# Kernel optimization log

Measured on AMD Instinct MI355X. Metric: run time of the kernel, lower is better.

## Reference

```python
import jax, jax.numpy as jnp
import numpy as np

S, T, B = 32, 64, 64          # sentences, tokens/sentence, batch
V, E, H, G, C = 32000, 128, 128, 128, 5  # vocab, embed, intra hid, inter hid, classes


def _gru_dir(x, h0, Wih, Whh, bih, bhh):
    # x: [T,B,D]; Wih: [3H,D]; Whh: [3H,H]  (PyTorch GRU gate order r,z,n)
    xg = jnp.einsum('tbd,gd->tbg', x, Wih) + bih  # precompute input gates [T,B,3H]
    def step(h, xt):
        gh = h @ Whh.T + bhh
        ir, iz, inn = jnp.split(xt, 3, axis=-1)
        hr, hz, hn = jnp.split(gh, 3, axis=-1)
        r = jax.nn.sigmoid(ir + hr)
        z = jax.nn.sigmoid(iz + hz)
        n = jnp.tanh(inn + r * hn)
        hnew = (1 - z) * n + z * h
        return hnew, hnew
    _, out = jax.lax.scan(step, h0, xg)
    return out  # [T,B,H]


def _bigru(x, Wih, Whh, bih, bhh):
    # x: [T,B,D]; Wih: [2,3H,D] (fwd, bwd). Zero initial state (init_hidden()).
    h0 = jnp.zeros((x.shape[1], Whh.shape[-1]), x.dtype)
    of = _gru_dir(x, h0, Wih[0], Whh[0], bih[0], bhh[0])
    ob = _gru_dir(x[::-1], h0, Wih[1], Whh[1], bih[1], bhh[1])[::-1]
    return jnp.concatenate([of, ob], axis=-1)  # [T,B,2H]


def setup_inputs() -> dict:
    key = jax.random.key(0)
    ks = iter(jax.random.split(key, 20))
    u = lambda k, shp, s: jax.random.uniform(k, shp, jnp.float32, -s, s)
    tokens = jax.random.randint(next(ks), (S, T, B), 0, V)
    return {
        'tokens': tokens,
        'embed_table': jax.random.normal(next(ks), (V, E), jnp.float32),
        # intra biGRU (input E, hidden H)
        'Wih_intra': u(next(ks), (2, 3 * H, E), 0.08),
        'Whh_intra': u(next(ks), (2, 3 * H, H), 0.08),
        'bih_intra': u(next(ks), (2, 3 * H), 0.08),
        'bhh_intra': u(next(ks), (2, 3 * H), 0.08),
        # intra attention
        'W_W_intra': u(next(ks), (2 * H, 2 * H), 0.1),
        'b_intra': u(next(ks), (2 * H,), 0.1),
        'proj_intra': u(next(ks), (2 * H,), 0.1),
        # inter biGRU (input 2H, hidden G)
        'Wih_inter': u(next(ks), (2, 3 * G, 2 * H), 0.08),
        'Whh_inter': u(next(ks), (2, 3 * G, G), 0.08),
        'bih_inter': u(next(ks), (2, 3 * G), 0.08),
        'bhh_inter': u(next(ks), (2, 3 * G), 0.08),
        # inter attention
        'W_W_inter': u(next(ks), (2 * G, 2 * G), 0.1),
        'b_inter': u(next(ks), (2 * G,), 0.1),
        'proj_inter': u(next(ks), (2 * G,), 0.1),
        # final linear
        'W_final': u(next(ks), (C, 2 * G), 0.06),
        'b_final': u(next(ks), (C,), 0.06),
    }


def reference(tokens, embed_table, Wih_intra, Whh_intra, bih_intra, bhh_intra,
              W_W_intra, b_intra, proj_intra, Wih_inter, Whh_inter, bih_inter,
              bhh_inter, W_W_inter, b_inter, proj_inter, W_final, b_final):
    # ---- intra (word-level) per sentence, fresh zero state each sentence ----
    emb = embed_table[tokens]                                   # [S,T,B,E]
    intra_out = jax.vmap(
        lambda xs: _bigru(xs, Wih_intra, Whh_intra, bih_intra, bhh_intra)
    )(emb)                                                      # [S,T,B,2H]
    u1 = jnp.tanh(jnp.einsum('stbh,hk->stbk', intra_out, W_W_intra) + b_intra)
    a1 = jnp.einsum('stbk,k->stb', u1, proj_intra)              # [S,T,B]
    a1 = jax.nn.softmax(a1, axis=1)                             # softmax over tokens
    sent_vecs = jnp.einsum('stb,stbh->sbh', a1, intra_out)      # [S,B,2H]
    # ---- inter (sentence-level) ----
    inter_out = _bigru(sent_vecs, Wih_inter, Whh_inter, bih_inter, bhh_inter)  # [S,B,2G]
    u2 = jnp.tanh(jnp.einsum('sbh,hk->sbk', inter_out, W_W_inter) + b_inter)
    a2 = jnp.einsum('sbk,k->sb', u2, proj_inter)                # NO softmax (faithful to source)
    doc_vec = jnp.einsum('sb,sbh->bh', a2, inter_out)           # [B,2G]
    final_map = doc_vec @ W_final.T + b_final                   # [B,C]
    return final_map
```

## Files before the change

### kernel.cpp

```cpp
#include <hip/hip_runtime.h>

#define S_ 32
#define T_ 64
#define B_ 64
#define V_ 32000
#define E_ 128
#define H_ 128
#define G_ 128
#define C_ 5

typedef short s8v __attribute__((ext_vector_type(8)));
typedef __bf16 b8v __attribute__((ext_vector_type(8)));
typedef float f32x4 __attribute__((ext_vector_type(4)));

template <typename V>
__device__ inline auto mfma_sel(V a, V b, f32x4 c, int)
    -> decltype(__builtin_amdgcn_mfma_f32_16x16x32_bf16(a, b, c, 0, 0, 0)) {
  return __builtin_amdgcn_mfma_f32_16x16x32_bf16(a, b, c, 0, 0, 0);
}
template <typename V>
__device__ inline f32x4 mfma_sel(V a, V b, f32x4 c, long) {
  return __builtin_amdgcn_mfma_f32_16x16x32_bf16(
      __builtin_bit_cast(b8v, a), __builtin_bit_cast(b8v, b), c, 0, 0, 0);
}
__device__ inline f32x4 mfma16(s8v a, s8v b, f32x4 c) { return mfma_sel(a, b, c, 0); }

__device__ inline float b2f(unsigned short u) {
  union { unsigned int i; float f; } v; v.i = ((unsigned int)u) << 16; return v.f;
}
__device__ inline unsigned short f2b(float f) {
  union { float f; unsigned int i; } v; v.f = f;
  return (unsigned short)((v.i + 0x8000u) >> 16);
}
__device__ inline unsigned short f2b_rne(float f) {
  union { float f; unsigned int i; } v; v.f = f;
  unsigned int r = (v.i + 0x7fffu + ((v.i >> 16) & 1u)) >> 16;
  return (unsigned short)r;
}
__device__ inline s8v cvt8(const float* p) {
  const float4 a = *(const float4*)p;
  const float4 b = *(const float4*)(p + 4);
  s8v r;
  r[0] = (short)f2b_rne(a.x); r[1] = (short)f2b_rne(a.y);
  r[2] = (short)f2b_rne(a.z); r[3] = (short)f2b_rne(a.w);
  r[4] = (short)f2b_rne(b.x); r[5] = (short)f2b_rne(b.y);
  r[6] = (short)f2b_rne(b.z); r[7] = (short)f2b_rne(b.w);
  return r;
}
__device__ inline float fsigm(float x) {
  return __builtin_amdgcn_rcpf(1.f + __builtin_amdgcn_exp2f(-1.44269504f * x));
}
__device__ inline float ftanh(float x) {
  return 1.f - 2.f * __builtin_amdgcn_rcpf(1.f + __builtin_amdgcn_exp2f(2.88539008f * x));
}

__device__ inline void lds_barrier() {
  asm volatile("s_waitcnt lgkmcnt(0)\n\ts_barrier" ::: "memory");
}

__global__ __launch_bounds__(256) void k_gtab(
    const float* __restrict__ emb,
    const float* __restrict__ wih,
    const float* __restrict__ bih,
    const float* __restrict__ bhh,
    const float* __restrict__ wwi,
    const float* __restrict__ wihI,
    unsigned short* __restrict__ gtab,
    unsigned short* __restrict__ wta,
    unsigned short* __restrict__ wib)
{
  __shared__ __align__(16) unsigned short res[64 * 776];
  __shared__ __align__(16) unsigned short alds[64 * 136];
  const int bid = blockIdx.x, tid = threadIdx.x;
  if (bid >= 504) {
    const int cb = bid - 504;
    for (int i = 0; i < 48; ++i) {
      int e4 = cb * 12288 + i * 256 + tid;
      float4 v = *(const float4*)&wihI[(size_t)e4 * 4];
      ushort4 u;
      u.x = f2b_rne(v.x); u.y = f2b_rne(v.y); u.z = f2b_rne(v.z); u.w = f2b_rne(v.w);
      *(ushort4*)&wib[(size_t)e4 * 4] = u;
    }
    return;
  }
  if (bid >= 500) {
    const int n0 = (bid - 500) * 64;
    for (int i = 0; i < 64; ++i) {
      int cid = i * 256 + tid;
      int k = cid >> 6, nl = cid & 63;
      res[nl * 264 + k] = f2b_rne(wwi[k * 256 + n0 + nl]);
    }
    __syncthreads();
    for (int i = 0; i < 8; ++i) {
      int cid = i * 256 + tid;
      int nl = cid >> 5, k8 = cid & 31;
      *(int4*)&wta[(size_t)(n0 + nl) * 256 + k8 * 8] =
          *(const int4*)&res[nl * 264 + k8 * 8];
    }
    return;
  }
  const int vbase = bid * 64;
  for (int i = 0; i < 8; ++i) {
    int cid = i * 256 + tid;
    int row = cid >> 5, kc = cid & 31;
    float4 v = *(const float4*)&emb[(size_t)(vbase + row) * 128 + kc * 4];
    ushort4 u;
    u.x = f2b_rne(v.x); u.y = f2b_rne(v.y); u.z = f2b_rne(v.z); u.w = f2b_rne(v.w);
    *(ushort4*)&alds[row * 136 + kc * 4] = u;
  }
  __syncthreads();
  const int w = tid >> 6, l = tid & 63, q = l >> 4, ln = l & 15;
  s8v af[4][4];
  for (int mt = 0; mt < 4; ++mt)
    for (int kf = 0; kf < 4; ++kf)
      af[mt][kf] = *(const s8v*)&alds[(mt * 16 + ln) * 136 + kf * 32 + q * 8];
  for (int nchunk = 0; nchunk < 6; ++nchunk) {
    const int nbase = nchunk * 128;
    s8v bf[2][4];
    float bias[2];
    for (int nt = 0; nt < 2; ++nt) {
      int c = nbase + (w * 2 + nt) * 16 + ln;
      int g = (c < 384) ? c : (c - 384);
      bias[nt] = bih[c] + (g < 256 ? bhh[c] : 0.f);
      for (int kf = 0; kf < 4; ++kf)
        bf[nt][kf] = cvt8(&wih[(size_t)c * 128 + kf * 32 + q * 8]);
    }
    for (int mt = 0; mt < 4; ++mt) {
      for (int nt = 0; nt < 2; ++nt) {
        f32x4 acc = {0.f, 0.f, 0.f, 0.f};
        for (int kf = 0; kf < 4; ++kf) acc = mfma16(af[mt][kf], bf[nt][kf], acc);
        const int col = nbase + (w * 2 + nt) * 16 + ln;
        for (int r = 0; r < 4; ++r) {
          const int row = mt * 16 + q * 4 + r;
          res[row * 776 + col] = f2b_rne(acc[r] + bias[nt]);
        }
      }
    }
  }
  __syncthreads();
  for (int i = 0; i < 24; ++i) {
    int cid = i * 256 + tid;
    int row = cid / 96, kc = cid - row * 96;
    *(int4*)&gtab[(size_t)(vbase + row) * 768 + kc * 8] =
        *(const int4*)&res[row * 776 + kc * 8];
  }
}

__global__ __launch_bounds__(512) void k_intra(
    const int* __restrict__ tokens,
    const unsigned short* __restrict__ gtab,
    const float* __restrict__ whh,
    const float* __restrict__ bhh,
    unsigned short* __restrict__ iout)
{
  const int bid = blockIdx.x;
  const int s = bid >> 3, dir = (bid >> 2) & 1, bq = bid & 3;
  const int bbase = bq * 16;
  const int tid = threadIdx.x;
  const int w = tid >> 6, l = tid & 63, q = l >> 4, ln = l & 15;
  const int gbase = w * 16, g0 = gbase + q * 4;

  __shared__ __align__(16) unsigned short hb[2][16 * 136];
  __shared__ __align__(16) unsigned short xbuf[2][16 * 392];
  __shared__ int tokl[T_ * 16];

  for (int i = tid; i < 2 * 16 * 136; i += 512) ((unsigned short*)hb)[i] = 0;
  for (int i = tid; i < T_ * 16; i += 512) {
    int t = i >> 4, bl = i & 15;
    tokl[i] = tokens[(s * T_ + t) * B_ + bbase + bl] * 768 + dir * 384;
  }

  s8v af[3][4];
  float hbn[4];
  const float* whd = whh + (size_t)dir * (384 * 128);
  const float* bhd = bhh + dir * 384;
  for (int g3 = 0; g3 < 3; ++g3)
    for (int kf = 0; kf < 4; ++kf)
      af[g3][kf] = cvt8(&whd[(size_t)(g3 * 128 + gbase + ln) * 128 + kf * 32 + q * 8]);
  for (int r = 0; r < 4; ++r) hbn[r] = bhd[256 + gbase + q * 4 + r];
  float h[4] = {0.f, 0.f, 0.f, 0.f};

  const bool stager = (w < 6);
  int sr0 = 0, sof0 = 0, sd0 = 0, sr1 = 0, sof1 = 0, sd1 = 0;
  {
    int e0 = w * 1024 + l * 8;
    int e1 = e0 + 512;
    sr0 = e0 / 384; sof0 = e0 - sr0 * 384; sd0 = sr0 * 392 + sof0;
    sr1 = e1 / 384; sof1 = e1 - sr1 * 384; sd1 = sr1 * 392 + sof1;
  }
  int4 ldA, ldB;
#define XLOAD(st)                                                           \
  do {                                                                      \
    int tt_ = (st) > (T_ - 1) ? (T_ - 1) : (st);                            \
    int tg_ = dir ? (T_ - 1 - tt_) : tt_;                                   \
    ldA = *(const int4*)&gtab[(size_t)tokl[tg_ * 16 + sr0] + sof0];         \
    ldB = *(const int4*)&gtab[(size_t)tokl[tg_ * 16 + sr1] + sof1];         \
  } while (0)
#define XWRITE(sl)                                                          \
  do {                                                                      \
    *(int4*)&xbuf[sl][sd0] = ldA;                                           \
    *(int4*)&xbuf[sl][sd1] = ldB;                                           \
  } while (0)

  __syncthreads();
  if (stager) {
    XLOAD(0);
    XWRITE(0);
    XLOAD(1);
  }
  __syncthreads();

  const int xb = ln * 392 + gbase + q * 4;
  int p = 0;
  int tprev = 0;
  for (int step = 0; step < T_; ++step) {
    const int t = dir ? (T_ - 1 - step) : step;
    const int sl = step & 1;
    if (stager) {
      XWRITE(sl ^ 1);
      XLOAD(step + 2);
    }
    if (step > 0 && tid < 256) {
      int row = tid >> 4, kc = tid & 15;
      int4 v = *(const int4*)&hb[p][row * 136 + kc * 8];
      *(int4*)&iout[((size_t)(s * T_ + tprev) * B_ + bbase + row) * 256 +
                    dir * 128 + kc * 8] = v;
    }
    s8v bfr[4];
    for (int kf = 0; kf < 4; ++kf)
      bfr[kf] = *(const s8v*)&hb[p][ln * 136 + kf * 32 + q * 8];
    f32x4 c0 = {0.f, 0.f, 0.f, 0.f}, c1 = c0, c2 = c0;
    for (int kf = 0; kf < 4; ++kf) {
      c0 = mfma16(af[0][kf], bfr[kf], c0);
      c1 = mfma16(af[1][kf], bfr[kf], c1);
      c2 = mfma16(af[2][kf], bfr[kf], c2);
    }
    const ushort4 xr = *(const ushort4*)&xbuf[sl][xb];
    const ushort4 xz = *(const ushort4*)&xbuf[sl][xb + 128];
    const ushort4 xn = *(const ushort4*)&xbuf[sl][xb + 256];
    const unsigned short* xrp = (const unsigned short*)&xr;
    const unsigned short* xzp = (const unsigned short*)&xz;
    const unsigned short* xnp = (const unsigned short*)&xn;
    unsigned short hnb[4];
    for (int r = 0; r < 4; ++r) {
      float rr = fsigm(b2f(xrp[r]) + c0[r]);
      float zz = fsigm(b2f(xzp[r]) + c1[r]);
      float nn = ftanh(b2f(xnp[r]) + rr * (c2[r] + hbn[r]));
      float hv = zz * (h[r] - nn) + nn;
      h[r] = hv;
      hnb[r] = f2b(hv);
    }
    ushort4 hv4; hv4.x = hnb[0]; hv4.y = hnb[1]; hv4.z = hnb[2]; hv4.w = hnb[3];
    *(ushort4*)&hb[p ^ 1][ln * 136 + g0] = hv4;
    lds_barrier();
    p ^= 1;
    tprev = t;
  }
  if (tid < 256) {
    int row = tid >> 4, kc = tid & 15;
    int4 v = *(const int4*)&hb[p][row * 136 + kc * 8];
    *(int4*)&iout[((size_t)(s * T_ + tprev) * B_ + bbase + row) * 256 +
                  dir * 128 + kc * 8] = v;
  }
#undef XLOAD
#undef XWRITE
}

__global__ __launch_bounds__(512, 1) void k_attn(
    const unsigned short* __restrict__ iout,
    const unsigned short* __restrict__ wta,
    const float* __restrict__ bint,
    const float* __restrict__ proj,
    const unsigned short* __restrict__ wib,
    const float* __restrict__ bihI,
    const float* __restrict__ bhhI,
    float* __restrict__ xgi)
{
  __shared__ __align__(16) unsigned short wlds[256 * 256];
  __shared__ float lgbuf[8][16];
  __shared__ float lbuf[8][8];
  const int tid = threadIdx.x, bid = blockIdx.x;
  const int s = bid >> 3, b0 = (bid & 7) * 8;
  for (int i = 0; i < 16; ++i) {
    int cid = i * 512 + tid;
    int n = cid >> 5, kc = cid & 31;
    *(int4*)&wlds[n * 256 + ((kc ^ (n & 15)) << 3)] =
        *(const int4*)&wta[(size_t)n * 256 + kc * 8];
  }
  const int w = tid >> 6, l = tid & 63, q = l >> 4, ln = l & 15;
  float bbv[16], ppv[16];
  for (int nt = 0; nt < 16; ++nt) {
    bbv[nt] = bint[nt * 16 + ln];
    ppv[nt] = proj[nt * 16 + ln];
  }
  __syncthreads();

  float O[8][8];
  for (int kf = 0; kf < 8; ++kf)
    for (int j = 0; j < 8; ++j) O[kf][j] = 0.f;
  float l_acc = 0.f;

  for (int tile = 0; tile < 4; ++tile) {
    const int t = (w * 4 + tile) * 2 + (ln >> 3);
    const size_t row = (size_t)((s * T_ + t) * B_ + b0 + (ln & 7));
    s8v af[8];
    for (int kf = 0; kf < 8; ++kf)
      af[kf] = *(const s8v*)&iout[row * 256 + kf * 32 + q * 8];
    float p0 = 0.f, p1 = 0.f, p2 = 0.f, p3 = 0.f;
    for (int nt = 0; nt < 16; ++nt) {
      f32x4 c = {0.f, 0.f, 0.f, 0.f};
      for (int kf = 0; kf < 8; ++kf) {
        s8v bf = *(const s8v*)&wlds[(nt * 16 + ln) * 256 + (((kf * 4 + q) ^ ln) << 3)];
        c = mfma16(af[kf], bf, c);
      }
      p0 += ppv[nt] * ftanh(c[0] + bbv[nt]);
      p1 += ppv[nt] * ftanh(c[1] + bbv[nt]);
      p2 += ppv[nt] * ftanh(c[2] + bbv[nt]);
      p3 += ppv[nt] * ftanh(c[3] + bbv[nt]);
    }
    for (int d = 1; d < 16; d <<= 1) {
      p0 += __shfl_xor(p0, d); p1 += __shfl_xor(p1, d);
      p2 += __shfl_xor(p2, d); p3 += __shfl_xor(p3, d);
    }
    if (ln == 0) {
      lgbuf[w][q * 4 + 0] = p0; lgbuf[w][q * 4 + 1] = p1;
      lgbuf[w][q * 4 + 2] = p2; lgbuf[w][q * 4 + 3] = p3;
    }
    const float lg = lgbuf[w][ln];
    const float e = __builtin_amdgcn_exp2f(1.44269504f * lg);
    l_acc += e;
    for (int kf = 0; kf < 8; ++kf)
      for (int j = 0; j < 8; ++j)
        O[kf][j] += e * b2f((unsigned short)af[kf][j]);
  }
  l_acc += __shfl_xor(l_acc, 8);
  for (int kf = 0; kf < 8; ++kf)
    for (int j = 0; j < 8; ++j) O[kf][j] += __shfl_xor(O[kf][j], 8);
  __syncthreads();
  float* obuf = (float*)wlds;
  unsigned short* svl = (unsigned short*)(((char*)wlds) + 65536);
  if (ln < 8) {
    const int base = w * 2048 + ln * 256 + q * 8;
    for (int kf = 0; kf < 8; ++kf) {
      float4 v0; v0.x = O[kf][0]; v0.y = O[kf][1]; v0.z = O[kf][2]; v0.w = O[kf][3];
      float4 v1; v1.x = O[kf][4]; v1.y = O[kf][5]; v1.z = O[kf][6]; v1.w = O[kf][7];
      *(float4*)&obuf[base + kf * 32]     = v0;
      *(float4*)&obuf[base + kf * 32 + 4] = v1;
    }
    if (q == 0) lbuf[w][ln] = l_acc;
  }
  {
    ushort4 z4; z4.x = 0; z4.y = 0; z4.z = 0; z4.w = 0;
    int rr = 8 + (tid >> 6), cc = (tid & 63) * 4;
    *(ushort4*)&svl[rr * 264 + cc] = z4;
  }
  __syncthreads();
  const int idx = tid * 4;
  const int bb_ = idx >> 8;
  float4 acc; acc.x = 0.f; acc.y = 0.f; acc.z = 0.f; acc.w = 0.f;
  float lsum = 0.f;
  for (int w8 = 0; w8 < 8; ++w8) {
    const float4 v = *(const float4*)&obuf[w8 * 2048 + idx];
    acc.x += v.x; acc.y += v.y; acc.z += v.z; acc.w += v.w;
    lsum += lbuf[w8][bb_];
  }
  const float inv = __builtin_amdgcn_rcpf(lsum);
  ushort4 u;
  u.x = f2b_rne(acc.x * inv); u.y = f2b_rne(acc.y * inv);
  u.z = f2b_rne(acc.z * inv); u.w = f2b_rne(acc.w * inv);
  *(ushort4*)&svl[bb_ * 264 + (idx & 255)] = u;
  __syncthreads();
  s8v afx[8];
  for (int kf = 0; kf < 8; ++kf)
    afx[kf] = *(const s8v*)&svl[ln * 264 + kf * 32 + q * 8];
  for (int nt = 0; nt < 6; ++nt) {
    const int c = w * 96 + nt * 16 + ln;
    const int dirI = (c >= 384) ? 1 : 0;
    const int g = c - dirI * 384;
    const float biasx = bihI[c] + (g < 256 ? bhhI[c] : 0.f);
    f32x4 cacc = {0.f, 0.f, 0.f, 0.f};
    for (int kf = 0; kf < 8; ++kf) {
      s8v bfx = *(const s8v*)&wib[(size_t)c * 256 + kf * 32 + q * 8];
      cacc = mfma16(afx[kf], bfx, cacc);
    }
    if (q < 2) {
      for (int r = 0; r < 4; ++r) {
        const int m = q * 4 + r;
        xgi[((size_t)dirI * 2048 + s * B_ + b0 + m) * 384 + g] = cacc[r] + biasx;
      }
    }
  }
}

__global__ __launch_bounds__(512) void k_inter(
    const float* __restrict__ xgi,
    const float* __restrict__ whh,
    const float* __restrict__ bhh,
    float* __restrict__ io2)
{
  const int bid = blockIdx.x;
  const int dir = bid >> 2, bq = bid & 3, bbase = bq * 16;
  const int tid = threadIdx.x;
  const int w = tid >> 6, l = tid & 63, q = l >> 4, ln = l & 15;
  const int gbase = w * 16, g0 = gbase + q * 4;
  __shared__ __align__(16) unsigned short hb[2][16 * 136];
  for (int i = tid; i < 2 * 16 * 136; i += 512) ((unsigned short*)hb)[i] = 0;
  s8v af[3][4];
  float hbn[4];
  const float* whd = whh + (size_t)dir * (384 * 128);
  const float* bhd = bhh + dir * 384;
  for (int g3 = 0; g3 < 3; ++g3) {
    const int R = g3 * 128 + gbase;
    for (int kf = 0; kf < 4; ++kf)
      af[g3][kf] = cvt8(&whd[(size_t)(R + ln) * 128 + kf * 32 + q * 8]);
  }
  for (int r = 0; r < 4; ++r) hbn[r] = bhd[256 + gbase + q * 4 + r];
  float h[4] = {0.f, 0.f, 0.f, 0.f};
  const int b = bbase + ln;
  __syncthreads();

  float4 Vr[4], Vz[4], Vn[4];
#define GLOAD_S(slot, st)                                                   \
  do {                                                                      \
    int tt_ = (st) > (S_ - 1) ? (S_ - 1) : (st);                            \
    int sg_ = dir ? (S_ - 1 - tt_) : tt_;                                   \
    const float* xp_ = xgi + ((size_t)dir * 2048 + sg_ * 64 + b) * 384 + g0;\
    Vr[slot] = *(const float4*)&xp_[0];                                     \
    Vz[slot] = *(const float4*)&xp_[128];                                   \
    Vn[slot] = *(const float4*)&xp_[256];                                   \
  } while (0)

  GLOAD_S(0, 0);
  GLOAD_S(1, 1);
  GLOAD_S(2, 2);

  int p = 0;
  for (int it = 0; it < S_ / 4; ++it) {
#pragma unroll
    for (int j = 0; j < 4; ++j) {
      const int step = it * 4 + j;
      const int sI = dir ? (S_ - 1 - step) : step;
      GLOAD_S((j + 3) & 3, step + 3);

      s8v bfr[4];
      for (int kf = 0; kf < 4; ++kf)
        bfr[kf] = *(const s8v*)&hb[p][ln * 136 + kf * 32 + q * 8];
      f32x4 c0 = {0.f, 0.f, 0.f, 0.f}, c1 = c0, c2 = c0;
      for (int kf = 0; kf < 4; ++kf) {
        c0 = mfma16(af[0][kf], bfr[kf], c0);
        c1 = mfma16(af[1][kf], bfr[kf], c1);
        c2 = mfma16(af[2][kf], bfr[kf], c2);
      }
      const float irv[4] = {Vr[j].x, Vr[j].y, Vr[j].z, Vr[j].w};
      const float izv[4] = {Vz[j].x, Vz[j].y, Vz[j].z, Vz[j].w};
      const float inv[4] = {Vn[j].x, Vn[j].y, Vn[j].z, Vn[j].w};
      unsigned short hnb[4];
      for (int r = 0; r < 4; ++r) {
        float rr = fsigm(irv[r] + c0[r]);
        float zz = fsigm(izv[r] + c1[r]);
        float nn = ftanh(inv[r] + rr * (c2[r] + hbn[r]));
        float hv = zz * (h[r] - nn) + nn;
        h[r] = hv;
        hnb[r] = f2b(hv);
      }
      ushort4 hv4; hv4.x = hnb[0]; hv4.y = hnb[1]; hv4.z = hnb[2]; hv4.w = hnb[3];
      *(ushort4*)&hb[p ^ 1][ln * 136 + g0] = hv4;
      float4 of4; of4.x = h[0]; of4.y = h[1]; of4.z = h[2]; of4.w = h[3];
      *(float4*)&io2[((size_t)(sI * 64 + b)) * 256 + dir * 128 + g0] = of4;
      lds_barrier();
      p ^= 1;
    }
  }
#undef GLOAD_S
}

__global__ __launch_bounds__(256) void k_attn_i(
    const float* __restrict__ io2,
    const float* __restrict__ wwI,
    const float* __restrict__ bI,
    const float* __restrict__ projI,
    float* __restrict__ a2)
{
  const int bid = blockIdx.x, tid = threadIdx.x;
  const int r0 = bid * 8;
  __shared__ float iol[8 * 256];
  __shared__ float red[4 * 8];
  for (int i = 0; i < 8; ++i) iol[i * 256 + tid] = io2[(size_t)(r0 + i) * 256 + tid];
  __syncthreads();
  float acc[8];
  for (int i = 0; i < 8; ++i) acc[i] = 0.f;
  for (int hh = 0; hh < 256; ++hh) {
    const float wv = wwI[hh * 256 + tid];
    for (int i = 0; i < 8; ++i) acc[i] += wv * iol[i * 256 + hh];
  }
  const float bb = bI[tid], pp = projI[tid];
  float p[8];
  for (int i = 0; i < 8; ++i) p[i] = pp * ftanh(acc[i] + bb);
  for (int d = 1; d < 64; d <<= 1)
    for (int i = 0; i < 8; ++i) p[i] += __shfl_xor(p[i], d);
  const int w = tid >> 6, l = tid & 63;
  if (l == 0)
    for (int i = 0; i < 8; ++i) red[w * 8 + i] = p[i];
  __syncthreads();
  if (tid < 8) a2[r0 + tid] = red[tid] + red[8 + tid] + red[16 + tid] + red[24 + tid];
}

__global__ __launch_bounds__(256) void k_final(
    const float* __restrict__ a2,
    const float* __restrict__ io2,
    const float* __restrict__ wf,
    const float* __restrict__ bfi,
    float* __restrict__ out)
{
  const int b = blockIdx.x, tid = threadIdx.x;
  __shared__ float av[S_];
  __shared__ float dv[256];
  __shared__ float red[4];
  if (tid < S_) av[tid] = a2[tid * 64 + b];
  __syncthreads();
  float acc = 0.f;
  for (int s = 0; s < S_; ++s) acc += av[s] * io2[((size_t)(s * 64 + b)) * 256 + tid];
  dv[tid] = acc;
  __syncthreads();
  for (int c = 0; c < C_; ++c) {
    float pv = wf[c * 256 + tid] * dv[tid];
    for (int d = 1; d < 64; d <<= 1) pv += __shfl_xor(pv, d);
    const int w = tid >> 6, l = tid & 63;
    if (l == 0) red[w] = pv;
    __syncthreads();
    if (tid == 0)
      out[b * C_ + c] = red[0] + red[1] + red[2] + red[3] + bfi[c];
    __syncthreads();
  }
}

extern "C" void kernel_launch(void* const* d_in, const int* in_sizes, int n_in,
                              void* d_out, int out_size, void* d_ws, size_t ws_size,
                              hipStream_t stream) {
  (void)in_sizes; (void)n_in; (void)out_size; (void)ws_size;
  const int*   tokens = (const int*)d_in[0];
  const float* emb    = (const float*)d_in[1];
  const float* wih_a  = (const float*)d_in[2];
  const float* whh_a  = (const float*)d_in[3];
  const float* bih_a  = (const float*)d_in[4];
  const float* bhh_a  = (const float*)d_in[5];
  const float* ww_a   = (const float*)d_in[6];
  const float* b_a    = (const float*)d_in[7];
  const float* proj_a = (const float*)d_in[8];
  const float* wih_i  = (const float*)d_in[9];
  const float* whh_i  = (const float*)d_in[10];
  const float* bih_i  = (const float*)d_in[11];
  const float* bhh_i  = (const float*)d_in[12];
  const float* ww_i   = (const float*)d_in[13];
  const float* b_i    = (const float*)d_in[14];
  const float* proj_i = (const float*)d_in[15];
  const float* w_fin  = (const float*)d_in[16];
  const float* b_fin  = (const float*)d_in[17];

  char* ws = (char*)d_ws;
  unsigned short* gtab = (unsigned short*)(ws + 0);
  unsigned short* wta  = (unsigned short*)(ws + 49152000);
  unsigned short* iout = (unsigned short*)(ws + 49283072);
  unsigned short* wib  = (unsigned short*)(ws + 116391936);
  float* xgi = (float*)(ws + 119537664);
  float* io2 = (float*)(ws + 125829120);
  float* a2  = (float*)(ws + 127926272);

  k_gtab<<<508, 256, 0, stream>>>(emb, wih_a, bih_a, bhh_a, ww_a, wih_i,
                                  gtab, wta, wib);
  k_intra<<<256, 512, 0, stream>>>(tokens, gtab, whh_a, bhh_a, iout);
  k_attn<<<256, 512, 0, stream>>>(iout, wta, b_a, proj_a, wib, bih_i, bhh_i, xgi);
  k_inter<<<8, 512, 0, stream>>>(xgi, whh_i, bhh_i, io2);
  k_attn_i<<<256, 256, 0, stream>>>(io2, ww_i, b_i, proj_i, a2);
  k_final<<<64, 256, 0, stream>>>(a2, io2, w_fin, b_fin, (float*)d_out);
}
```

Measured before the change: 294.8 us.

## Fuse attention, inter GRU, inter attention and final into one persistent kernel

Merges the four post-intra kernels into a single 256-block kernel that separates stages with software grid barriers built on atomic counters in workspace. The counters are reset by the preceding intra kernel. This removes three kernel launches and their inter-kernel gaps. In exchange it relies on all 256 blocks being co-resident, and it adds spin-wait overhead while 248 blocks idle during the serial inter GRU.

Result: slower. 619.3 us (+110.1%).

```diff
diff --git a/kernel.cpp b/kernel.cpp
--- a/kernel.cpp
+++ b/kernel.cpp
@@ -8,6 +8,7 @@
 #define H_ 128
 #define G_ 128
 #define C_ 5
+#define NB_ 256
 
 typedef short s8v __attribute__((ext_vector_type(8)));
 typedef __bf16 b8v __attribute__((ext_vector_type(8)));
@@ -56,6 +57,17 @@
 
 __device__ inline void lds_barrier() {
   asm volatile("s_waitcnt lgkmcnt(0)\n\ts_barrier" ::: "memory");
+}
+
+__device__ inline void gsync(int* c) {
+  __syncthreads();
+  if (threadIdx.x == 0) {
+    __threadfence();
+    atomicAdd(c, 1);
+    while (atomicAdd(c, 0) < NB_) __builtin_amdgcn_s_sleep(16);
+    __threadfence();
+  }
+  __syncthreads();
 }
 
 __global__ __launch_bounds__(256) void k_gtab(
@@ -151,12 +163,14 @@
     const unsigned short* __restrict__ gtab,
     const float* __restrict__ whh,
     const float* __restrict__ bhh,
-    unsigned short* __restrict__ iout)
+    unsigned short* __restrict__ iout,
+    int* __restrict__ gctr)
 {
   const int bid = blockIdx.x;
   const int s = bid >> 3, dir = (bid >> 2) & 1, bq = bid & 3;
   const int bbase = bq * 16;
   const int tid = threadIdx.x;
+  if (bid == 0 && tid < 4) gctr[tid] = 0;
   const int w = tid >> 6, l = tid & 63, q = l >> 4, ln = l & 15;
   const int gbase = w * 16, g0 = gbase + q * 4;
 
@@ -266,7 +280,7 @@
 #undef XWRITE
 }
 
-__global__ __launch_bounds__(512, 1) void k_attn(
+__global__ __launch_bounds__(512, 1) void k_mega(
     const unsigned short* __restrict__ iout,
     const unsigned short* __restrict__ wta,
     const float* __restrict__ bint,
@@ -274,263 +288,264 @@
     const unsigned short* __restrict__ wib,
     const float* __restrict__ bihI,
     const float* __restrict__ bhhI,
-    float* __restrict__ xgi)
+    float* __restrict__ xgi,
+    const float* __restrict__ whhI,
+    float* __restrict__ io2,
+    const float* __restrict__ wwI,
+    const float* __restrict__ bI,
+    const float* __restrict__ projI,
+    const float* __restrict__ wf,
+    const float* __restrict__ bfi,
+    float* __restrict__ a2,
+    int* __restrict__ gctr,
+    float* __restrict__ out)
 {
   __shared__ __align__(16) unsigned short wlds[256 * 256];
   __shared__ float lgbuf[8][16];
   __shared__ float lbuf[8][8];
   const int tid = threadIdx.x, bid = blockIdx.x;
-  const int s = bid >> 3, b0 = (bid & 7) * 8;
-  for (int i = 0; i < 16; ++i) {
-    int cid = i * 512 + tid;
-    int n = cid >> 5, kc = cid & 31;
-    *(int4*)&wlds[n * 256 + ((kc ^ (n & 15)) << 3)] =
-        *(const int4*)&wta[(size_t)n * 256 + kc * 8];
-  }
-  const int w = tid >> 6, l = tid & 63, q = l >> 4, ln = l & 15;
-  float bbv[16], ppv[16];
-  for (int nt = 0; nt < 16; ++nt) {
-    bbv[nt] = bint[nt * 16 + ln];
-    ppv[nt] = proj[nt * 16 + ln];
-  }
-  __syncthreads();
-
-  float O[8][8];
-  for (int kf = 0; kf < 8; ++kf)
-    for (int j = 0; j < 8; ++j) O[kf][j] = 0.f;
-  float l_acc = 0.f;
-
-  for (int tile = 0; tile < 4; ++tile) {
-    const int t = (w * 4 + tile) * 2 + (ln >> 3);
-    const size_t row = (size_t)((s * T_ + t) * B_ + b0 + (ln & 7));
-    s8v af[8];
+
+  {
+    const int s = bid >> 3, b0 = (bid & 7) * 8;
+    for (int i = 0; i < 16; ++i) {
+      int cid = i * 512 + tid;
+      int n = cid >> 5, kc = cid & 31;
+      *(int4*)&wlds[n * 256 + ((kc ^ (n & 15)) << 3)] =
+          *(const int4*)&wta[(size_t)n * 256 + kc * 8];
+    }
+    const int w = tid >> 6, l = tid & 63, q = l >> 4, ln = l & 15;
+    float bbv[16], ppv[16];
+    for (int nt = 0; nt < 16; ++nt) {
+      bbv[nt] = bint[nt * 16 + ln];
+      ppv[nt] = proj[nt * 16 + ln];
+    }
+    __syncthreads();
+
+    float O[8][8];
     for (int kf = 0; kf < 8; ++kf)
-      af[kf] = *(const s8v*)&iout[row * 256 + kf * 32 + q * 8];
-    float p0 = 0.f, p1 = 0.f, p2 = 0.f, p3 = 0.f;
-    for (int nt = 0; nt < 16; ++nt) {
-      f32x4 c = {0.f, 0.f, 0.f, 0.f};
+      for (int j = 0; j < 8; ++j) O[kf][j] = 0.f;
+    float l_acc = 0.f;
+
+    for (int tile = 0; tile < 4; ++tile) {
+      const int t = (w * 4 + tile) * 2 + (ln >> 3);
+      const size_t row = (size_t)((s * T_ + t) * B_ + b0 + (ln & 7));
+      s8v af[8];
+      for (int kf = 0; kf < 8; ++kf)
+        af[kf] = *(const s8v*)&iout[row * 256 + kf * 32 + q * 8];
+      float p0 = 0.f, p1 = 0.f, p2 = 0.f, p3 = 0.f;
+      for (int nt = 0; nt < 16; ++nt) {
+        f32x4 c = {0.f, 0.f, 0.f, 0.f};
+        for (int kf = 0; kf < 8; ++kf) {
+          s8v bf = *(const s8v*)&wlds[(nt * 16 + ln) * 256 + (((kf * 4 + q) ^ ln) << 3)];
+          c = mfma16(af[kf], bf, c);
+        }
+        p0 += ppv[nt] * ftanh(c[0] + bbv[nt]);
+        p1 += ppv[nt] * ftanh(c[1] + bbv[nt]);
+        p2 += ppv[nt] * ftanh(c[2] + bbv[nt]);
+        p3 += ppv[nt] * ftanh(c[3] + bbv[nt]);
+      }
+      for (int d = 1; d < 16; d <<= 1) {
+        p0 += __shfl_xor(p0, d); p1 += __shfl_xor(p1, d);
+        p2 += __shfl_xor(p2, d); p3 += __shfl_xor(p3, d);
+      }
+      if (ln == 0) {
+        lgbuf[w][q * 4 + 0] = p0; lgbuf[w][q * 4 + 1] = p1;
+        lgbuf[w][q * 4 + 2] = p2; lgbuf[w][q * 4 + 3] = p3;
+      }
+      const float lg = lgbuf[w][ln];
+      const float e = __builtin_amdgcn_exp2f(1.44269504f * lg);
+      l_acc += e;
+      for (int kf = 0; kf < 8; ++kf)
+        for (int j = 0; j < 8; ++j)
+          O[kf][j] += e * b2f((unsigned short)af[kf][j]);
+    }
+    l_acc += __shfl_xor(l_acc, 8);
+    for (int kf = 0; kf < 8; ++kf)
+      for (int j = 0; j < 8; ++j) O[kf][j] += __shfl_xor(O[kf][j], 8);
+    __syncthreads();
+    float* obuf = (float*)wlds;
+    unsigned short* svl = (unsigned short*)(((char*)wlds) + 65536);
+    if (ln < 8) {
+      const int base = w * 2048 + ln * 256 + q * 8;
       for (int kf = 0; kf < 8; ++kf) {
-        s8v bf = *(const s8v*)&wlds[(nt * 16 + ln) * 256 + (((kf * 4 + q) ^ ln) << 3)];
-        c = mfma16(af[kf], bf, c);
-      }
-      p0 += ppv[nt] * ftanh(c[0] + bbv[nt]);
-      p1 += ppv[nt] * ftanh(c[1] + bbv[nt]);
-      p2 += ppv[nt] * ftanh(c[2] + bbv[nt]);
-      p3 += ppv[nt] * ftanh(c[3] + bbv[nt]);
-    }
-    for (int d = 1; d < 16; d <<= 1) {
-      p0 += __shfl_xor(p0, d); p1 += __shfl_xor(p1, d);
-      p2 += __shfl_xor(p2, d); p3 += __shfl_xor(p3, d);
-    }
-    if (ln == 0) {
-      lgbuf[w][q * 4 + 0] = p0; lgbuf[w][q * 4 + 1] = p1;
-      lgbuf[w][q * 4 + 2] = p2; lgbuf[w][q * 4 + 3] = p3;
-    }
-    const float lg = lgbuf[w][ln];
-    const float e = __builtin_amdgcn_exp2f(1.44269504f * lg);
-    l_acc += e;
+        float4 v0; v0.x = O[kf][0]; v0.y = O[kf][1]; v0.z = O[kf][2]; v0.w = O[kf][3];
+        float4 v1; v1.x = O[kf][4]; v1.y = O[kf][5]; v1.z = O[kf][6]; v1.w = O[kf][7];
+        *(float4*)&obuf[base + kf * 32]     = v0;
+        *(float4*)&obuf[base + kf * 32 + 4] = v1;
+      }
+      if (q == 0) lbuf[w][ln] = l_acc;
+    }
+    {
+      ushort4 z4; z4.x = 0; z4.y = 0; z4.z = 0; z4.w = 0;
+      int rr = 8 + (tid >> 6), cc = (tid & 63) * 4;
+      *(ushort4*)&svl[rr * 264 + cc] = z4;
+    }
+    __syncthreads();
+    const int idx = tid * 4;
+    const int bb_ = idx >> 8;
+    float4 acc; acc.x = 0.f; acc.y = 0.f; acc.z = 0.f; acc.w = 0.f;
+    float lsum = 0.f;
+    for (int w8 = 0; w8 < 8; ++w8) {
+      const float4 v = *(const float4*)&obuf[w8 * 2048 + idx];
+      acc.x += v.x; acc.y += v.y; acc.z += v.z; acc.w += v.w;
+      lsum += lbuf[w8][bb_];
+    }
+    const float inv = __builtin_amdgcn_rcpf(lsum);
+    ushort4 u;
+    u.x = f2b_rne(acc.x * inv); u.y = f2b_rne(acc.y * inv);
+    u.z = f2b_rne(acc.z * inv); u.w = f2b_rne(acc.w * inv);
+    *(ushort4*)&svl[bb_ * 264 + (idx & 255)] = u;
+    __syncthreads();
+    s8v afx[8];
     for (int kf = 0; kf < 8; ++kf)
-      for (int j = 0; j < 8; ++j)
-        O[kf][j] += e * b2f((unsigned short)af[kf][j]);
-  }
-  l_acc += __shfl_xor(l_acc, 8);
-  for (int kf = 0; kf < 8; ++kf)
-    for (int j = 0; j < 8; ++j) O[kf][j] += __shfl_xor(O[kf][j], 8);
-  __syncthreads();
-  float* obuf = (float*)wlds;
-  unsigned short* svl = (unsigned short*)(((char*)wlds) + 65536);
-  if (ln < 8) {
-    const int base = w * 2048 + ln * 256 + q * 8;
-    for (int kf = 0; kf < 8; ++kf) {
-      float4 v0; v0.x = O[kf][0]; v0.y = O[kf][1]; v0.z = O[kf][2]; v0.w = O[kf][3];
-      float4 v1; v1.x = O[kf][4]; v1.y = O[kf][5]; v1.z = O[kf][6]; v1.w = O[kf][7];
-      *(float4*)&obuf[base + kf * 32]     = v0;
-      *(float4*)&obuf[base + kf * 32 + 4] = v1;
-    }
-    if (q == 0) lbuf[w][ln] = l_acc;
-  }
+      afx[kf] = *(const s8v*)&svl[ln * 264 + kf * 32 + q * 8];
+    for (int nt = 0; nt < 6; ++nt) {
+      const int c = w * 96 + nt * 16 + ln;
+      const int dirI = (c >= 384) ? 1 : 0;
+      const int g = c - dirI * 384;
+      const float biasx = bihI[c] + (g < 256 ? bhhI[c] : 0.f);
+      f32x4 cacc = {0.f, 0.f, 0.f, 0.f};
+      for (int kf = 0; kf < 8; ++kf) {
+        s8v bfx = *(const s8v*)&wib[(size_t)c * 256 + kf * 32 + q * 8];
+        cacc = mfma16(afx[kf], bfx, cacc);
+      }
+      if (q < 2) {
+        for (int r = 0; r < 4; ++r) {
+          const int m = q * 4 + r;
+          xgi[((size_t)dirI * 2048 + s * B_ + b0 + m) * 384 + g] = cacc[r] + biasx;
+        }
+      }
+    }
+  }
+  gsync(gctr + 0);
+
+  if (bid < 8) {
+    unsigned short* hbB = wlds;
+    const int dir = bid >> 2, bq = bid & 3, bbase = bq * 16;
+    const int w = tid >> 6, l = tid & 63, q = l >> 4, ln = l & 15;
+    const int gbase = w * 16, g0 = gbase + q * 4;
+    for (int i = tid; i < 2 * 16 * 136; i += 512) hbB[i] = 0;
+    s8v af[3][4];
+    float hbn[4];
+    const float* whd = whhI + (size_t)dir * (384 * 128);
+    const float* bhd = bhhI + dir * 384;
+    for (int g3 = 0; g3 < 3; ++g3) {
+      const int R = g3 * 128 + gbase;
+      for (int kf = 0; kf < 4; ++kf)
+        af[g3][kf] = cvt8(&whd[(size_t)(R + ln) * 128 + kf * 32 + q * 8]);
+    }
+    for (int r = 0; r < 4; ++r) hbn[r] = bhd[256 + gbase + q * 4 + r];
+    float h[4] = {0.f, 0.f, 0.f, 0.f};
+    const int b = bbase + ln;
+    __syncthreads();
+
+    float4 Vr[4], Vz[4], Vn[4];
+#define GLOAD_S(slot, st)                                                   \
+    do {                                                                    \
+      int tt_ = (st) > (S_ - 1) ? (S_ - 1) : (st);                          \
+      int sg_ = dir ? (S_ - 1 - tt_) : tt_;                                 \
+      const float* xp_ = xgi + ((size_t)dir * 2048 + sg_ * 64 + b) * 384 + g0;\
+      Vr[slot] = *(const float4*)&xp_[0];                                   \
+      Vz[slot] = *(const float4*)&xp_[128];                                 \
+      Vn[slot] = *(const float4*)&xp_[256];                                 \
+    } while (0)
+
+    GLOAD_S(0, 0);
+    GLOAD_S(1, 1);
+    GLOAD_S(2, 2);
+
+    int p = 0;
+    for (int it = 0; it < S_ / 4; ++it) {
+#pragma unroll
+      for (int j = 0; j < 4; ++j) {
+        const int step = it * 4 + j;
+        const int sI = dir ? (S_ - 1 - step) : step;
+        GLOAD_S((j + 3) & 3, step + 3);
+
+        s8v bfr[4];
+        for (int kf = 0; kf < 4; ++kf)
+          bfr[kf] = *(const s8v*)&hbB[p * 2176 + ln * 136 + kf * 32 + q * 8];
+        f32x4 c0 = {0.f, 0.f, 0.f, 0.f}, c1 = c0, c2 = c0;
+        for (int kf = 0; kf < 4; ++kf) {
+          c0 = mfma16(af[0][kf], bfr[kf], c0);
+          c1 = mfma16(af[1][kf], bfr[kf], c1);
+          c2 = mfma16(af[2][kf], bfr[kf], c2);
+        }
+        const float irv[4] = {Vr[j].x, Vr[j].y, Vr[j].z, Vr[j].w};
+        const float izv[4] = {Vz[j].x, Vz[j].y, Vz[j].z, Vz[j].w};
+        const float inv[4] = {Vn[j].x, Vn[j].y, Vn[j].z, Vn[j].w};
+        unsigned short hnb[4];
+        for (int r = 0; r < 4; ++r) {
+          float rr = fsigm(irv[r] + c0[r]);
+          float zz = fsigm(izv[r] + c1[r]);
+          float nn = ftanh(inv[r] + rr * (c2[r] + hbn[r]));
+          float hv = zz * (h[r] - nn) + nn;
+          h[r] = hv;
+          hnb[r] = f2b(hv);
+        }
+        ushort4 hv4; hv4.x = hnb[0]; hv4.y = hnb[1]; hv4.z = hnb[2]; hv4.w = hnb[3];
+        *(ushort4*)&hbB[(p ^ 1) * 2176 + ln * 136 + g0] = hv4;
+        float4 of4; of4.x = h[0]; of4.y = h[1]; of4.z = h[2]; of4.w = h[3];
+        *(float4*)&io2[((size_t)(sI * 64 + b)) * 256 + dir * 128 + g0] = of4;
+        lds_barrier();
+        p ^= 1;
+      }
+    }
+#undef GLOAD_S
+  }
+  gsync(gctr + 1);
+
   {
-    ushort4 z4; z4.x = 0; z4.y = 0; z4.z = 0; z4.w = 0;
-    int rr = 8 + (tid >> 6), cc = (tid & 63) * 4;
-    *(ushort4*)&svl[rr * 264 + cc] = z4;
-  }
-  __syncthreads();
-  const int idx = tid * 4;
-  const int bb_ = idx >> 8;
-  float4 acc; acc.x = 0.f; acc.y = 0.f; acc.z = 0.f; acc.w = 0.f;
-  float lsum = 0.f;
-  for (int w8 = 0; w8 < 8; ++w8) {
-    const float4 v = *(const float4*)&obuf[w8 * 2048 + idx];
-    acc.x += v.x; acc.y += v.y; acc.z += v.z; acc.w += v.w;
-    lsum += lbuf[w8][bb_];
-  }
-  const float inv = __builtin_amdgcn_rcpf(lsum);
-  ushort4 u;
-  u.x = f2b_rne(acc.x * inv); u.y = f2b_rne(acc.y * inv);
-  u.z = f2b_rne(acc.z * inv); u.w = f2b_rne(acc.w * inv);
-  *(ushort4*)&svl[bb_ * 264 + (idx & 255)] = u;
-  __syncthreads();
-  s8v afx[8];
-  for (int kf = 0; kf < 8; ++kf)
-    afx[kf] = *(const s8v*)&svl[ln * 264 + kf * 32 + q * 8];
-  for (int nt = 0; nt < 6; ++nt) {
-    const int c = w * 96 + nt * 16 + ln;
-    const int dirI = (c >= 384) ? 1 : 0;
-    const int g = c - dirI * 384;
-    const float biasx = bihI[c] + (g < 256 ? bhhI[c] : 0.f);
-    f32x4 cacc = {0.f, 0.f, 0.f, 0.f};
-    for (int kf = 0; kf < 8; ++kf) {
-      s8v bfx = *(const s8v*)&wib[(size_t)c * 256 + kf * 32 + q * 8];
-      cacc = mfma16(afx[kf], bfx, cacc);
-    }
-    if (q < 2) {
-      for (int r = 0; r < 4; ++r) {
-        const int m = q * 4 + r;
-        xgi[((size_t)dirI * 2048 + s * B_ + b0 + m) * 384 + g] = cacc[r] + biasx;
-      }
-    }
-  }
-}
-
-__global__ __launch_bounds__(512) void k_inter(
-    const float* __restrict__ xgi,
-    const float* __restrict__ whh,
-    const float* __restrict__ bhh,
-    float* __restrict__ io2)
-{
-  const int bid = blockIdx.x;
-  const int dir = bid >> 2, bq = bid & 3, bbase = bq * 16;
-  const int tid = threadIdx.x;
-  const int w = tid >> 6, l = tid & 63, q = l >> 4, ln = l & 15;
-  const int gbase = w * 16, g0 = gbase + q * 4;
-  __shared__ __align__(16) unsigned short hb[2][16 * 136];
-  for (int i = tid; i < 2 * 16 * 136; i += 512) ((unsigned short*)hb)[i] = 0;
-  s8v af[3][4];
-  float hbn[4];
-  const float* whd = whh + (size_t)dir * (384 * 128);
-  const float* bhd = bhh + dir * 384;
-  for (int g3 = 0; g3 < 3; ++g3) {
-    const int R = g3 * 128 + gbase;
-    for (int kf = 0; kf < 4; ++kf)
-      af[g3][kf] = cvt8(&whd[(size_t)(R + ln) * 128 + kf * 32 + q * 8]);
-  }
-  for (int r = 0; r < 4; ++r) hbn[r] = bhd[256 + gbase + q * 4 + r];
-  float h[4] = {0.f, 0.f, 0.f, 0.f};
-  const int b = bbase + ln;
-  __syncthreads();
-
-  float4 Vr[4], Vz[4], Vn[4];
-#define GLOAD_S(slot, st)                                                   \
-  do {                                                                      \
-    int tt_ = (st) > (S_ - 1) ? (S_ - 1) : (st);                            \
-    int sg_ = dir ? (S_ - 1 - tt_) : tt_;                                   \
-    const float* xp_ = xgi + ((size_t)dir * 2048 + sg_ * 64 + b) * 384 + g0;\
-    Vr[slot] = *(const float4*)&xp_[0];                                     \
-    Vz[slot] = *(const float4*)&xp_[128];                                   \
-    Vn[slot] = *(const float4*)&xp_[256];                                   \
-  } while (0)
-
-  GLOAD_S(0, 0);
-  GLOAD_S(1, 1);
-  GLOAD_S(2, 2);
-
-  int p = 0;
-  for (int it = 0; it < S_ / 4; ++it) {
-#pragma unroll
-    for (int j = 0; j < 4; ++j) {
-      const int step = it * 4 + j;
-      const int sI = dir ? (S_ - 1 - step) : step;
-      GLOAD_S((j + 3) & 3, step + 3);
-
-      s8v bfr[4];
-      for (int kf = 0; kf < 4; ++kf)
-        bfr[kf] = *(const s8v*)&hb[p][ln * 136 + kf * 32 + q * 8];
-      f32x4 c0 = {0.f, 0.f, 0.f, 0.f}, c1 = c0, c2 = c0;
-      for (int kf = 0; kf < 4; ++kf) {
-        c0 = mfma16(af[0][kf], bfr[kf], c0);
-        c1 = mfma16(af[1][kf], bfr[kf], c1);
-        c2 = mfma16(af[2][kf], bfr[kf], c2);
-      }
-      const float irv[4] = {Vr[j].x, Vr[j].y, Vr[j].z, Vr[j].w};
-      const float izv[4] = {Vz[j].x, Vz[j].y, Vz[j].z, Vz[j].w};
-      const float inv[4] = {Vn[j].x, Vn[j].y, Vn[j].z, Vn[j].w};
-      unsigned short hnb[4];
-      for (int r = 0; r < 4; ++r) {
-        float rr = fsigm(irv[r] + c0[r]);
-        float zz = fsigm(izv[r] + c1[r]);
-        float nn = ftanh(inv[r] + rr * (c2[r] + hbn[r]));
-        float hv = zz * (h[r] - nn) + nn;
-        h[r] = hv;
-        hnb[r] = f2b(hv);
-      }
-      ushort4 hv4; hv4.x = hnb[0]; hv4.y = hnb[1]; hv4.z = hnb[2]; hv4.w = hnb[3];
-      *(ushort4*)&hb[p ^ 1][ln * 136 + g0] = hv4;
-      float4 of4; of4.x = h[0]; of4.y = h[1]; of4.z = h[2]; of4.w = h[3];
-      *(float4*)&io2[((size_t)(sI * 64 + b)) * 256 + dir * 128 + g0] = of4;
-      lds_barrier();
-      p ^= 1;
-    }
-  }
-#undef GLOAD_S
-}
-
-__global__ __launch_bounds__(256) void k_attn_i(
-    const float* __restrict__ io2,
-    const float* __restrict__ wwI,
-    const float* __restrict__ bI,
-    const float* __restrict__ projI,
-    float* __restrict__ a2)
-{
-  const int bid = blockIdx.x, tid = threadIdx.x;
-  const int r0 = bid * 8;
-  __shared__ float iol[8 * 256];
-  __shared__ float red[4 * 8];
-  for (int i = 0; i < 8; ++i) iol[i * 256 + tid] = io2[(size_t)(r0 + i) * 256 + tid];
-  __syncthreads();
-  float acc[8];
-  for (int i = 0; i < 8; ++i) acc[i] = 0.f;
-  for (int hh = 0; hh < 256; ++hh) {
-    const float wv = wwI[hh * 256 + tid];
-    for (int i = 0; i < 8; ++i) acc[i] += wv * iol[i * 256 + hh];
-  }
-  const float bb = bI[tid], pp = projI[tid];
-  float p[8];
-  for (int i = 0; i < 8; ++i) p[i] = pp * ftanh(acc[i] + bb);
-  for (int d = 1; d < 64; d <<= 1)
-    for (int i = 0; i < 8; ++i) p[i] += __shfl_xor(p[i], d);
-  const int w = tid >> 6, l = tid & 63;
-  if (l == 0)
-    for (int i = 0; i < 8; ++i) red[w * 8 + i] = p[i];
-  __syncthreads();
-  if (tid < 8) a2[r0 + tid] = red[tid] + red[8 + tid] + red[16 + tid] + red[24 + tid];
-}
-
-__global__ __launch_bounds__(256) void k_final(
-    const float* __restrict__ a2,
-    const float* __restrict__ io2,
-    const float* __restrict__ wf,
-    const float* __restrict__ bfi,
-    float* __restrict__ out)
-{
-  const int b = blockIdx.x, tid = threadIdx.x;
-  __shared__ float av[S_];
-  __shared__ float dv[256];
-  __shared__ float red[4];
-  if (tid < S_) av[tid] = a2[tid * 64 + b];
-  __syncthreads();
-  float acc = 0.f;
-  for (int s = 0; s < S_; ++s) acc += av[s] * io2[((size_t)(s * 64 + b)) * 256 + tid];
-  dv[tid] = acc;
-  __syncthreads();
-  for (int c = 0; c < C_; ++c) {
-    float pv = wf[c * 256 + tid] * dv[tid];
-    for (int d = 1; d < 64; d <<= 1) pv += __shfl_xor(pv, d);
-    const int w = tid >> 6, l = tid & 63;
-    if (l == 0) red[w] = pv;
-    __syncthreads();
-    if (tid == 0)
-      out[b * C_ + c] = red[0] + red[1] + red[2] + red[3] + bfi[c];
-    __syncthreads();
+    float* iol = (float*)wlds;
+    float* redC = (float*)(((char*)wlds) + 8192);
+    const int r0 = bid * 8;
+    for (int i = tid; i < 8 * 256; i += 512)
+      iol[i] = io2[(size_t)r0 * 256 + i];
+    __syncthreads();
+    const int k = tid & 255, half = tid >> 8;
+    float acc[4];
+    for (int i = 0; i < 4; ++i) acc[i] = 0.f;
+    for (int hh = 0; hh < 256; ++hh) {
+      const float wv = wwI[hh * 256 + k];
+      for (int i = 0; i < 4; ++i) acc[i] += wv * iol[(half * 4 + i) * 256 + hh];
+    }
+    const float bb = bI[k], pp = projI[k];
+    float pv[4];
+    for (int i = 0; i < 4; ++i) pv[i] = pp * ftanh(acc[i] + bb);
+    for (int d = 1; d < 64; d <<= 1)
+      for (int i = 0; i < 4; ++i) pv[i] += __shfl_xor(pv[i], d);
+    const int wv_ = tid >> 6, l_ = tid & 63;
+    if (l_ == 0)
+      for (int i = 0; i < 4; ++i) redC[wv_ * 4 + i] = pv[i];
+    __syncthreads();
+    if (tid < 8) {
+      const int h4 = tid >> 2, i = tid & 3;
+      a2[r0 + h4 * 4 + i] = redC[(h4 * 4 + 0) * 4 + i] + redC[(h4 * 4 + 1) * 4 + i] +
+                            redC[(h4 * 4 + 2) * 4 + i] + redC[(h4 * 4 + 3) * 4 + i];
+    }
+  }
+  gsync(gctr + 2);
+
+  if (bid < 64) {
+    const int b = bid;
+    float* avD  = (float*)wlds;
+    float* red2 = avD + 32;
+    if (tid < S_) avD[tid] = a2[tid * 64 + b];
+    __syncthreads();
+    float dv = 0.f;
+    if (tid < 256) {
+      for (int ss = 0; ss < S_; ++ss)
+        dv += avD[ss] * io2[((size_t)(ss * 64 + b)) * 256 + tid];
+    }
+    for (int c = 0; c < C_; ++c) {
+      float pvv = (tid < 256) ? wf[c * 256 + tid] * dv : 0.f;
+      for (int d = 1; d < 64; d <<= 1) pvv += __shfl_xor(pvv, d);
+      if (tid < 256 && (tid & 63) == 0) red2[tid >> 6] = pvv;
+      __syncthreads();
+      if (tid == 0)
+        out[b * C_ + c] = red2[0] + red2[1] + red2[2] + red2[3] + bfi[c];
+      __syncthreads();
+    }
   }
 }
 
@@ -565,12 +580,12 @@
   float* xgi = (float*)(ws + 119537664);
   float* io2 = (float*)(ws + 125829120);
   float* a2  = (float*)(ws + 127926272);
+  int*   gctr = (int*)(ws + 127934464);
 
   k_gtab<<<508, 256, 0, stream>>>(emb, wih_a, bih_a, bhh_a, ww_a, wih_i,
                                   gtab, wta, wib);
-  k_intra<<<256, 512, 0, stream>>>(tokens, gtab, whh_a, bhh_a, iout);
-  k_attn<<<256, 512, 0, stream>>>(iout, wta, b_a, proj_a, wib, bih_i, bhh_i, xgi);
-  k_inter<<<8, 512, 0, stream>>>(xgi, whh_i, bhh_i, io2);
-  k_attn_i<<<256, 256, 0, stream>>>(io2, ww_i, b_i, proj_i, a2);
-  k_final<<<64, 256, 0, stream>>>(a2, io2, w_fin, b_fin, (float*)d_out);
-}
+  k_intra<<<256, 512, 0, stream>>>(tokens, gtab, whh_a, bhh_a, iout, gctr);
+  k_mega<<<256, 512, 0, stream>>>(iout, wta, b_a, proj_a, wib, bih_i, bhh_i,
+                                  xgi, whh_i, io2, ww_i, b_i, proj_i,
+                                  w_fin, b_fin, a2, gctr, (float*)d_out);
+}
```
